# Performance work log

Hardware: AMD Instinct MI355X
Metric: run time of the kernel (lower is better)

Reference implementation:

```python
import jax, jax.numpy as jnp
import numpy as np

N = 4000; T_GRU = 32; T_TREE = 16; F = 256; HS = 128; H = 3 * HS; CC = 512; E = 64000; D4 = 4 * HS


def _gru_last(x, wi, wh, bi, bh):
    # x: [N, T, F]; torch GRU gate order r, z, n. Returns last hidden [N, H].
    xp = jnp.einsum('ntf,gf->ntg', x, wi) + bi  # [N, T, 3H]
    h0 = jnp.zeros((x.shape[0], wh.shape[1]), x.dtype)
    def step(h, xt):
        gh = h @ wh.T + bh
        ir, iz, inn = jnp.split(xt, 3, axis=1)
        hr, hz, hn = jnp.split(gh, 3, axis=1)
        r = jax.nn.sigmoid(ir + hr)
        z = jax.nn.sigmoid(iz + hz)
        n = jnp.tanh(inn + r * hn)
        return (1.0 - z) * n + z * h, None
    hT, _ = jax.lax.scan(step, h0, jnp.swapaxes(xp, 0, 1))
    return hT


def _tree_root(x, ioux_w, ioux_b, iouh_w, iouh_b, fx_w, fx_b, fh_w, fh_b):
    # Chain-structured TreeLSTM (each node has one child); x: [N, T, F], leaf-to-root.
    xi = jnp.einsum('ntf,gf->ntg', x, ioux_w) + ioux_b  # [N, T, 3M]
    xf = jnp.einsum('ntf,mf->ntm', x, fx_w) + fx_b      # [N, T, M]
    M = fh_w.shape[0]
    z0 = jnp.zeros((x.shape[0], M), x.dtype)
    def step(carry, xs):
        c, h = carry
        xi_t, xf_t = xs
        iou = xi_t + h @ iouh_w.T + iouh_b
        i, o, u = jnp.split(iou, 3, axis=1)
        f = jax.nn.sigmoid(xf_t + h @ fh_w.T + fh_b)
        c = jax.nn.sigmoid(i) * jnp.tanh(u) + f * c
        h = jax.nn.sigmoid(o) * jnp.tanh(c)
        return (c, h), None
    (c, h), _ = jax.lax.scan(step, (z0, z0), (jnp.swapaxes(xi, 0, 1), jnp.swapaxes(xf, 0, 1)))
    return h


def _gcn(x, w, b, row, col):
    # PyG GCNConv: self-loops + symmetric normalization.
    n = x.shape[0]
    xw = x @ w.T
    loops = jnp.arange(n, dtype=row.dtype)
    r = jnp.concatenate([row, loops])
    c = jnp.concatenate([col, loops])
    deg = jax.ops.segment_sum(jnp.ones(r.shape, x.dtype), c, num_segments=n)
    dinv = jnp.where(deg > 0, jax.lax.rsqrt(jnp.maximum(deg, 1e-12)), 0.0)
    norm = (dinv[r] * dinv[c])[:, None]
    return jax.ops.segment_sum(xw[r] * norm, c, num_segments=n) + b


def setup_inputs() -> dict:
    key = jax.random.key(0)
    ks = jax.random.split(key, 48)
    s = 0.05
    p = lambda i, sh: jax.random.normal(ks[i], sh, jnp.float32) * s
    return {
        'feat1': p(0, (N, T_GRU, F)),
        'feat2': p(1, (N, T_TREE, F)),
        'feat3': p(2, (N, T_TREE, F)),
        'feat4': p(3, (N, CC)),
        'edge_index': jax.random.randint(ks[4], (2, E), 0, N),
        'gru_wi': p(5, (3 * H, F)), 'gru_wh': p(6, (3 * H, H)),
        'gru_bi': p(7, (3 * H,)), 'gru_bh': p(8, (3 * H,)),
        't1_ioux_w': p(9, (3 * H, F)), 't1_ioux_b': p(10, (3 * H,)),
        't1_iouh_w': p(11, (3 * H, H)), 't1_iouh_b': p(12, (3 * H,)),
        't1_fx_w': p(13, (H, F)), 't1_fx_b': p(14, (H,)),
        't1_fh_w': p(15, (H, H)), 't1_fh_b': p(16, (H,)),
        't2_ioux_w': p(17, (3 * H, F)), 't2_ioux_b': p(18, (3 * H,)),
        't2_iouh_w': p(19, (3 * H, H)), 't2_iouh_b': p(20, (3 * H,)),
        't2_fx_w': p(21, (H, F)), 't2_fx_b': p(22, (H,)),
        't2_fh_w': p(23, (H, H)), 't2_fh_b': p(24, (H,)),
        'r1_w': p(25, (HS, H)), 'r1_b': p(26, (HS,)),
        'r2_w': p(27, (HS, H)), 'r2_b': p(28, (HS,)),
        'r3_w': p(29, (HS, H)), 'r3_b': p(30, (HS,)),
        'r4_w': p(31, (HS, CC)), 'r4_b': p(32, (HS,)),
        'gcn0_w': p(33, (D4, D4)), 'gcn0_b': p(34, (D4,)),
        'gcn1_w': p(35, (D4, D4)), 'gcn1_b': p(36, (D4,)),
        'r7_w': p(37, (2, D4)), 'r7_b': p(38, (2,)),
    }


def reference(feat1, feat2, feat3, feat4, edge_index,
              gru_wi, gru_wh, gru_bi, gru_bh,
              t1_ioux_w, t1_ioux_b, t1_iouh_w, t1_iouh_b, t1_fx_w, t1_fx_b, t1_fh_w, t1_fh_b,
              t2_ioux_w, t2_ioux_b, t2_iouh_w, t2_iouh_b, t2_fx_w, t2_fx_b, t2_fh_w, t2_fh_b,
              r1_w, r1_b, r2_w, r2_b, r3_w, r3_b, r4_w, r4_b,
              gcn0_w, gcn0_b, gcn1_w, gcn1_b, r7_w, r7_b):
    v1 = _gru_last(feat1, gru_wi, gru_wh, gru_bi, gru_bh)            # [N, H]
    v2 = _tree_root(feat2, t1_ioux_w, t1_ioux_b, t1_iouh_w, t1_iouh_b, t1_fx_w, t1_fx_b, t1_fh_w, t1_fh_b)
    v3 = _tree_root(feat3, t2_ioux_w, t2_ioux_b, t2_iouh_w, t2_iouh_b, t2_fx_w, t2_fx_b, t2_fh_w, t2_fh_b)
    f1 = v1 @ r1_w.T + r1_b
    f2 = v2 @ r2_w.T + r2_b
    f3 = v3 @ r3_w.T + r3_b
    f4 = feat4 @ r4_w.T + r4_b
    m = jnp.concatenate([f1, f2, f3, f4], axis=1)                    # [N, 4*HS]
    row, col = edge_index[0], edge_index[1]
    m = jax.nn.relu(_gcn(m, gcn0_w, gcn0_b, row, col))
    m = _gcn(m, gcn1_w, gcn1_b, row, col)
    m = jax.nn.softmax(m @ r7_w.T + r7_b, axis=1)                    # [N, 2]
    return m.T                                                       # [2, N]
```

## Files before the change

### kernel.cpp

```cpp
#include <hip/hip_runtime.h>
#include <hip/hip_bf16.h>
#include <math.h>

#define NN 4000
#define TG 32
#define TT 16
#define FF 256
#define HH 384
#define GCOLS 1536
#define KCAT 640
#define EE 64000
#define D4 512

typedef __attribute__((ext_vector_type(8))) short short8;
typedef __attribute__((ext_vector_type(4))) float float4v;

static __device__ __forceinline__ float fsig(float x)  { return 1.0f / (1.0f + __expf(-x)); }
static __device__ __forceinline__ float ftanh(float x) { return 2.0f / (1.0f + __expf(-2.0f*x)) - 1.0f; }
static __device__ __forceinline__ unsigned short f2bf(float f) {
    __hip_bfloat16 h = __float2bfloat16(f); return *reinterpret_cast<unsigned short*>(&h);
}

static __device__ __forceinline__ void async_copy16(const void* g, void* l) {
    __builtin_amdgcn_global_load_lds(
        (const __attribute__((address_space(1))) unsigned int*)g,
        (__attribute__((address_space(3))) unsigned int*)l, 16, 0, 0);
}

static __device__ __forceinline__ void xcd_swz(int& bx, int& by, int& bz) {
    const int gx = gridDim.x, gy = gridDim.y;
    const int nwg = gx * gy * gridDim.z;
    const int w = (blockIdx.z * gy + blockIdx.y) * gx + blockIdx.x;
    const int q = nwg >> 3, r = nwg & 7;
    const int xcd = w & 7, i = w >> 3;
    const int L = (xcd < r ? xcd*(q+1) : r*(q+1) + (xcd - r)*q) + i;
    bx = L % gx; int rest = L / gx;
    by = rest % gy; bz = rest / gy;
}

__global__ __launch_bounds__(256) void prep_w_kernel(
    const float* __restrict__ gwi, const float* __restrict__ gwh,
    const float* __restrict__ gbi, const float* __restrict__ gbh,
    const float* __restrict__ x1w, const float* __restrict__ x1b,
    const float* __restrict__ h1w, const float* __restrict__ h1b,
    const float* __restrict__ fx1w, const float* __restrict__ fx1b,
    const float* __restrict__ fh1w, const float* __restrict__ fh1b,
    const float* __restrict__ x2w, const float* __restrict__ x2b,
    const float* __restrict__ h2w, const float* __restrict__ h2b,
    const float* __restrict__ fx2w, const float* __restrict__ fx2b,
    const float* __restrict__ fh2w, const float* __restrict__ fh2b,
    __hip_bfloat16* __restrict__ Wx, __hip_bfloat16* __restrict__ Wh,
    float* __restrict__ bp)
{
    int z = blockIdx.z;
    int idx = blockIdx.x * 256 + threadIdx.x;
    int c = idx / KCAT, k = idx - c * KCAT;
    int bx = c >> 7, wc = (c >> 6) & 1, g = (c >> 4) & 3, rl = c & 15;
    int j = bx*32 + wc*16 + rl;
    float v = 0.0f, bv = 0.0f;
    if (z == 0) {
        if (g <= 1) {
            int row = g*HH + j;
            v = (k < FF) ? gwi[row*FF + k] : gwh[row*HH + (k-FF)];
            bv = gbi[row] + gbh[row];
        } else if (g == 2) {
            int row = 2*HH + j;
            v = (k < FF) ? gwi[row*FF + k] : 0.0f;
            bv = gbi[row];
        } else {
            int row = 2*HH + j;
            v = (k < FF) ? 0.0f : gwh[row*HH + (k-FF)];
            bv = gbh[row];
        }
    } else {
        const float* xw  = (z==1)? x1w  : x2w;   const float* xb  = (z==1)? x1b  : x2b;
        const float* hw  = (z==1)? h1w  : h2w;   const float* hb_ = (z==1)? h1b  : h2b;
        const float* fxw = (z==1)? fx1w : fx2w;  const float* fxb = (z==1)? fx1b : fx2b;
        const float* fhw = (z==1)? fh1w : fh2w;  const float* fhb = (z==1)? fh1b : fh2b;
        if (g < 3) {
            int row = g*HH + j;
            v = (k < FF) ? xw[row*FF + k] : hw[row*HH + (k-FF)];
            bv = xb[row] + hb_[row];
        } else {
            v = (k < FF) ? fxw[j*FF + k] : fhw[j*HH + (k-FF)];
            bv = fxb[j] + fhb[j];
        }
    }
    if (k < FF) Wx[(size_t)z*GCOLS*FF + (size_t)c*FF + k] = __float2bfloat16(v);
    else        Wh[(size_t)z*GCOLS*HH + (size_t)c*HH + (k-FF)] = __float2bfloat16(v);
    if (k == 0) bp[z*GCOLS + c] = bv;
}

__global__ __launch_bounds__(256) void f2b4_kernel(const float* __restrict__ s,
                                                   __hip_bfloat16* __restrict__ d, int n4)
{
    int i = blockIdx.x*256 + threadIdx.x;
    if (i >= n4) return;
    float4 v = ((const float4*)s)[i];
    ushort4 u = { f2bf(v.x), f2bf(v.y), f2bf(v.z), f2bf(v.w) };
    ((ushort4*)d)[i] = u;
}

#define BM 128
#define BN 128
#define BKK 32

__global__ __launch_bounds__(256) void gemm0_k(
    const __hip_bfloat16* __restrict__ Ab, size_t zA, int lda,
    const __hip_bfloat16* __restrict__ Wb, size_t zW, int K,
    const float* __restrict__ bias, size_t zB,
    float* __restrict__ C, size_t zC,
    __hip_bfloat16* __restrict__ C16, size_t zC16,
    int ldC, int M)
{
    const int z = blockIdx.z;
    const __hip_bfloat16* A = Ab + zA*z;
    const __hip_bfloat16* W = Wb + zW*z;

    __shared__ __align__(16) __hip_bfloat16 As[BM][BKK];
    __shared__ __align__(16) __hip_bfloat16 Bs[BN][BKK];

    const int tid  = threadIdx.x;
    const int lane = tid & 63;
    const int w    = tid >> 6;
    const int wr = w >> 1, wc = w & 1;
    const int rowBase = blockIdx.y * BM;
    const int colBase = blockIdx.x * BN;
    const int sRow = tid >> 2;
    const int sK   = (tid & 3) * 8;

    float4v acc[4][4];
    #pragma unroll
    for (int i = 0; i < 4; ++i)
        #pragma unroll
        for (int j = 0; j < 4; ++j)
            acc[i][j] = (float4v){0.f, 0.f, 0.f, 0.f};

    const int rl = lane & 15;
    const int kl = (lane >> 4) * 8;

    for (int kt = 0; kt < K; kt += BKK) {
        const int kk = kt + sK;
        #pragma unroll
        for (int i = 0; i < 2; ++i) {
            int gr = rowBase + i*64 + sRow;
            if (gr > M-1) gr = M-1;
            async_copy16(A + (size_t)gr*lda + kk, &As[i*64 + sRow][sK]);
        }
        #pragma unroll
        for (int i = 0; i < 2; ++i) {
            int r = i*64 + sRow;
            async_copy16(W + (size_t)(colBase + r)*K + kk, &Bs[r][sK]);
        }
        __syncthreads();

        short8 af[4], bfr[4];
        #pragma unroll
        for (int mi = 0; mi < 4; ++mi)
            af[mi] = *(const short8*)&As[wr*64 + mi*16 + rl][kl];
        #pragma unroll
        for (int ni = 0; ni < 4; ++ni)
            bfr[ni] = *(const short8*)&Bs[wc*64 + ni*16 + rl][kl];
        #pragma unroll
        for (int mi = 0; mi < 4; ++mi)
            #pragma unroll
            for (int ni = 0; ni < 4; ++ni)
                acc[mi][ni] = __builtin_amdgcn_mfma_f32_16x16x32_bf16(af[mi], bfr[ni], acc[mi][ni], 0, 0, 0);
        __syncthreads();
    }

    const int rq = (lane >> 4) * 4;
    float* Cz = C + zC*z;
    __hip_bfloat16* C16z = C16 ? (C16 + zC16*z) : nullptr;
    #pragma unroll
    for (int mi = 0; mi < 4; ++mi) {
        #pragma unroll
        for (int q = 0; q < 4; ++q) {
            int row = rowBase + wr*64 + mi*16 + rq + q;
            if (row >= M) continue;
            #pragma unroll
            for (int ni = 0; ni < 4; ++ni) {
                int col = colBase + wc*64 + ni*16 + rl;
                float v = acc[mi][ni][q];
                if (bias) v += bias[zB*z + col];
                Cz[(size_t)row*ldC + col] = v;
                if (C16z) C16z[(size_t)row*ldC + col] = __float2bfloat16(v);
            }
        }
    }
}

#define SBM 64
#define NT (KCAT/BKK)

struct StepSet {
    const __hip_bfloat16 *X, *Hin, *Wx, *Wh;
    const float *bp, *Sin;
    float *Sout;
    __hip_bfloat16 *Hout;
    int lda, xoff;
};

template<int MODE>
__global__ __launch_bounds__(256) void step_k(StepSet G, StepSet T)
{
    int bxi, byi, bzi;
    xcd_swz(bxi, byi, bzi);

    int mode, zt;
    if (MODE == 3 && bzi > 0) { mode = 2; zt = bzi - 1; }
    else { mode = 1; zt = 0; }
    const StepSet& S = (mode == 1) ? G : T;

    const __hip_bfloat16* X  = S.X   + (size_t)zt*TT*NN*FF;
    const __hip_bfloat16* Hi = S.Hin + (size_t)zt*NN*HH;
    const __hip_bfloat16* Wx = S.Wx  + (size_t)zt*GCOLS*FF;
    const __hip_bfloat16* Wh = S.Wh  + (size_t)zt*GCOLS*HH;
    const float* bp = S.bp + (size_t)zt*GCOLS;
    const float* Si = S.Sin + (size_t)zt*NN*HH;
    float* So = S.Sout + (size_t)zt*NN*HH;
    __hip_bfloat16* Ho = S.Hout + (size_t)zt*NN*HH;
    const int lda = S.lda, xoff = S.xoff;

    __shared__ __align__(16) __hip_bfloat16 As[4][SBM][BKK];
    __shared__ __align__(16) __hip_bfloat16 Bs[4][BN][BKK];

    const int tid  = threadIdx.x;
    const int lane = tid & 63;
    const int w    = tid >> 6;
    const int wr = w >> 1, wc = w & 1;
    const int rowBase = byi * SBM;
    const int colBase = bxi * BN;

    const int sR  = tid >> 2;
    const int sC  = tid & 3;
    const int sSw = sC ^ ((sR >> 1) & 3);
    int gra = rowBase + sR; if (gra > NN-1) gra = NN-1;

    auto stage = [&](int buf, int kt) {
        if (kt < FF) {
            const int kk = kt + sSw*8;
            async_copy16(X  + (size_t)gra*lda + xoff + kk,          &As[buf][sR][sC*8]);
            async_copy16(Wx + (size_t)(colBase + sR)*FF + kk,       &Bs[buf][sR][sC*8]);
            async_copy16(Wx + (size_t)(colBase + 64 + sR)*FF + kk,  &Bs[buf][64 + sR][sC*8]);
        } else {
            const int kk = kt - FF + sSw*8;
            async_copy16(Hi + (size_t)gra*HH + kk,                  &As[buf][sR][sC*8]);
            async_copy16(Wh + (size_t)(colBase + sR)*HH + kk,       &Bs[buf][sR][sC*8]);
            async_copy16(Wh + (size_t)(colBase + 64 + sR)*HH + kk,  &Bs[buf][64 + sR][sC*8]);
        }
    };

    float4v acc[2][4];
    #pragma unroll
    for (int i = 0; i < 2; ++i)
        #pragma unroll
        for (int j = 0; j < 4; ++j)
            acc[i][j] = (float4v){0.f, 0.f, 0.f, 0.f};

    const int rl = lane & 15;
    const int dF = (lane >> 4) ^ ((rl >> 1) & 3);

    stage(0, 0);
    stage(1, BKK);

    for (int it = 0; it < NT; ++it) {
        if (it < NT-1) asm volatile("s_waitcnt vmcnt(3)" ::: "memory");
        else           asm volatile("s_waitcnt vmcnt(0)" ::: "memory");
        __builtin_amdgcn_sched_barrier(0);
        __builtin_amdgcn_s_barrier();
        __builtin_amdgcn_sched_barrier(0);
        if (it + 2 < NT) stage((it+2)&3, (it+2)*BKK);
        __builtin_amdgcn_sched_barrier(0);

        const int cur = it & 3;
        short8 af[2], bfr[4];
        #pragma unroll
        for (int mi = 0; mi < 2; ++mi)
            af[mi] = *(const short8*)&As[cur][wr*32 + mi*16 + rl][dF*8];

        const bool xph = (it*BKK) < FF;
        if (mode == 2) {
            #pragma unroll
            for (int ni = 0; ni < 4; ++ni)
                bfr[ni] = *(const short8*)&Bs[cur][wc*64 + ni*16 + rl][dF*8];
            asm volatile("s_waitcnt lgkmcnt(0)" ::: "memory");
            __builtin_amdgcn_sched_barrier(0);
            #pragma unroll
            for (int mi = 0; mi < 2; ++mi)
                #pragma unroll
                for (int ni = 0; ni < 4; ++ni)
                    acc[mi][ni] = __builtin_amdgcn_mfma_f32_16x16x32_bf16(af[mi], bfr[ni], acc[mi][ni], 0, 0, 0);
        } else if (xph) {
            #pragma unroll
            for (int ni = 0; ni < 3; ++ni)
                bfr[ni] = *(const short8*)&Bs[cur][wc*64 + ni*16 + rl][dF*8];
            asm volatile("s_waitcnt lgkmcnt(0)" ::: "memory");
            __builtin_amdgcn_sched_barrier(0);
            #pragma unroll
            for (int mi = 0; mi < 2; ++mi)
                #pragma unroll
                for (int ni = 0; ni < 3; ++ni)
                    acc[mi][ni] = __builtin_amdgcn_mfma_f32_16x16x32_bf16(af[mi], bfr[ni], acc[mi][ni], 0, 0, 0);
        } else {
            bfr[0] = *(const short8*)&Bs[cur][wc*64 + 0*16 + rl][dF*8];
            bfr[1] = *(const short8*)&Bs[cur][wc*64 + 1*16 + rl][dF*8];
            bfr[3] = *(const short8*)&Bs[cur][wc*64 + 3*16 + rl][dF*8];
            asm volatile("s_waitcnt lgkmcnt(0)" ::: "memory");
            __builtin_amdgcn_sched_barrier(0);
            #pragma unroll
            for (int mi = 0; mi < 2; ++mi) {
                acc[mi][0] = __builtin_amdgcn_mfma_f32_16x16x32_bf16(af[mi], bfr[0], acc[mi][0], 0, 0, 0);
                acc[mi][1] = __builtin_amdgcn_mfma_f32_16x16x32_bf16(af[mi], bfr[1], acc[mi][1], 0, 0, 0);
                acc[mi][3] = __builtin_amdgcn_mfma_f32_16x16x32_bf16(af[mi], bfr[3], acc[mi][3], 0, 0, 0);
            }
        }
    }

    const int rq = (lane >> 4) * 4;
    const int j  = (colBase >> 2) + wc*16 + rl;
    const int cb = colBase + wc*64 + rl;
    float b0 = bp[cb + 0];
    float b1 = bp[cb + 16];
    float b2 = bp[cb + 32];
    float b3 = bp[cb + 48];

    #pragma unroll
    for (int mi = 0; mi < 2; ++mi) {
        #pragma unroll
        for (int q = 0; q < 4; ++q) {
            int row = rowBase + wr*32 + mi*16 + rq + q;
            if (row >= NN) continue;
            float g0 = acc[mi][0][q] + b0;
            float g1 = acc[mi][1][q] + b1;
            float g2 = acc[mi][2][q] + b2;
            float g3 = acc[mi][3][q] + b3;
            size_t off = (size_t)row*HH + j;
            if (mode == 1) {
                float r  = fsig(g0), zz = fsig(g1);
                float n  = ftanh(g2 + r*g3);
                float hp = Si[off];
                float hn = (1.0f - zz)*n + zz*hp;
                So[off] = hn;
                Ho[off] = __float2bfloat16(hn);
            } else {
                float cp = Si[off];
                float cn = fsig(g0)*ftanh(g2) + fsig(g3)*cp;
                So[off] = cn;
                float hn = fsig(g1)*ftanh(cn);
                Ho[off] = __float2bfloat16(hn);
            }
        }
    }
}

__global__ __launch_bounds__(256) void count_kernel(const int* __restrict__ col, int* __restrict__ degi)
{
    int e = blockIdx.x*256 + threadIdx.x;
    if (e < EE) atomicAdd(&degi[col[e]], 1);
}

__global__ __launch_bounds__(1024) void scan_kernel(const int* __restrict__ degi,
    int* __restrict__ start, int* __restrict__ cursor, float* __restrict__ dinv)
{
    __shared__ int s[1024];
    int t = threadIdx.x;
    int v[4]; int sum = 0;
    #pragma unroll
    for (int i = 0; i < 4; ++i) {
        int idx = t*4 + i;
        v[i] = (idx < NN) ? degi[idx] : 0;
        sum += v[i];
    }
    s[t] = sum;
    __syncthreads();
    for (int d = 1; d < 1024; d <<= 1) {
        int x = (t >= d) ? s[t-d] : 0;
        __syncthreads();
        s[t] += x;
        __syncthreads();
    }
    int base = s[t] - sum;
    int run = 0;
    #pragma unroll
    for (int i = 0; i < 4; ++i) {
        int idx = t*4 + i;
        if (idx < NN) {
            int st = base + run;
            start[idx] = st;
            cursor[idx] = st;
            dinv[idx] = rsqrtf((float)v[i] + 1.0f);
        }
        run += v[i];
    }
    if (t == 1023) start[NN] = s[1023];
}

__global__ __launch_bounds__(256) void fill_kernel(const int* __restrict__ row,
    const int* __restrict__ col, int* __restrict__ cursor, int* __restrict__ esrc)
{
    int e = blockIdx.x*256 + threadIdx.x;
    if (e < EE) {
        int c = col[e];
        int pos = atomicAdd(&cursor[c], 1);
        esrc[pos] = row[e];
    }
}

__global__ __launch_bounds__(256) void gather_kernel(const float* __restrict__ xw,
    const int* __restrict__ esrc, const int* __restrict__ start,
    const float* __restrict__ dinv, const float* __restrict__ bias,
    float* __restrict__ mout, __hip_bfloat16* __restrict__ mout16, int relu)
{
    int wv = threadIdx.x >> 6, lane = threadIdx.x & 63;
    int n = blockIdx.x*4 + wv;
    if (n >= NN) return;
    float a[8] = {0.f,0.f,0.f,0.f,0.f,0.f,0.f,0.f};
    int s0 = start[n], s1 = start[n+1];
    float dn = dinv[n];
    for (int e = s0; e < s1; ++e) {
        int r = esrc[e];
        float nrm = dinv[r]*dn;
        const float4 v0 = *(const float4*)(xw + (size_t)r*D4 + lane*8);
        const float4 v1 = *(const float4*)(xw + (size_t)r*D4 + lane*8 + 4);
        a[0] += v0.x*nrm; a[1] += v0.y*nrm; a[2] += v0.z*nrm; a[3] += v0.w*nrm;
        a[4] += v1.x*nrm; a[5] += v1.y*nrm; a[6] += v1.z*nrm; a[7] += v1.w*nrm;
    }
    const float4 u0 = *(const float4*)(xw + (size_t)n*D4 + lane*8);
    const float4 u1 = *(const float4*)(xw + (size_t)n*D4 + lane*8 + 4);
    float dd = dn*dn;
    float su[8] = {u0.x,u0.y,u0.z,u0.w,u1.x,u1.y,u1.z,u1.w};
    #pragma unroll
    for (int i = 0; i < 8; ++i) {
        float vv = a[i] + su[i]*dd + bias[lane*8 + i];
        if (relu) vv = fmaxf(vv, 0.0f);
        mout[(size_t)n*D4 + lane*8 + i] = vv;
        if (mout16) mout16[(size_t)n*D4 + lane*8 + i] = __float2bfloat16(vv);
    }
}

__global__ __launch_bounds__(256) void final_kernel(const float* __restrict__ m,
    const float* __restrict__ w, const float* __restrict__ b, float* __restrict__ out)
{
    int wave = threadIdx.x >> 6;
    int lane = threadIdx.x & 63;
    int n = blockIdx.x*4 + wave;
    const float* row = m + (size_t)n*D4 + lane*8;
    float4 v0 = *(const float4*)(row);
    float4 v1 = *(const float4*)(row + 4);
    const float* w0 = w + lane*8;
    const float* w1 = w + D4 + lane*8;
    float4 u0 = *(const float4*)(w0); float4 u1 = *(const float4*)(w0 + 4);
    float4 t0 = *(const float4*)(w1); float4 t1 = *(const float4*)(w1 + 4);
    float a = v0.x*u0.x + v0.y*u0.y + v0.z*u0.z + v0.w*u0.w
            + v1.x*u1.x + v1.y*u1.y + v1.z*u1.z + v1.w*u1.w;
    float bb = v0.x*t0.x + v0.y*t0.y + v0.z*t0.z + v0.w*t0.w
             + v1.x*t1.x + v1.y*t1.y + v1.z*t1.z + v1.w*t1.w;
    #pragma unroll
    for (int s = 32; s; s >>= 1) { a += __shfl_xor(a, s); bb += __shfl_xor(bb, s); }
    if (lane == 0) {
        float l0 = a + b[0], l1 = bb + b[1];
        float mx = fmaxf(l0, l1);
        float e0 = expf(l0 - mx), e1 = expf(l1 - mx);
        float s = e0 + e1;
        out[n]      = e0 / s;
        out[NN + n] = e1 / s;
    }
}

extern "C" void kernel_launch(void* const* d_in, const int* in_sizes, int n_in,
                              void* d_out, int out_size, void* d_ws, size_t ws_size,
                              hipStream_t stream)
{
    const float* feat1 = (const float*)d_in[0];
    const float* feat2 = (const float*)d_in[1];
    const float* feat3 = (const float*)d_in[2];
    const float* feat4 = (const float*)d_in[3];
    const int*   eidx  = (const int*)d_in[4];
    const float* r1w = (const float*)d_in[25]; const float* r1b = (const float*)d_in[26];
    const float* r2w = (const float*)d_in[27]; const float* r2b = (const float*)d_in[28];
    const float* r3w = (const float*)d_in[29]; const float* r3b = (const float*)d_in[30];
    const float* r4w = (const float*)d_in[31]; const float* r4b = (const float*)d_in[32];
    const float* g0w = (const float*)d_in[33]; const float* g0b = (const float*)d_in[34];
    const float* g1w = (const float*)d_in[35]; const float* g1b = (const float*)d_in[36];
    const float* r7w = (const float*)d_in[37]; const float* r7b = (const float*)d_in[38];

    float* ws = (float*)d_ws;
    size_t o = 0;
    auto alloc = [&](size_t nfl) { float* p = ws + o; o += (nfl + 3) & ~(size_t)3; return p; };

    float* hf0 = alloc((size_t)NN*HH);
    float* cf0 = alloc((size_t)2*NN*HH);
    __hip_bfloat16* hb0 = (__hip_bfloat16*)alloc((size_t)3*NN*HH/2);
    size_t zeroFloats = o;
    float* hf1 = alloc((size_t)NN*HH);
    float* cf1 = alloc((size_t)2*NN*HH);
    __hip_bfloat16* hb1 = (__hip_bfloat16*)alloc((size_t)3*NN*HH/2);
    __hip_bfloat16* xg  = (__hip_bfloat16*)alloc((size_t)TG*NN*FF/2);
    __hip_bfloat16* xt  = (__hip_bfloat16*)alloc((size_t)2*TT*NN*FF/2);
    __hip_bfloat16* Wx  = (__hip_bfloat16*)alloc((size_t)3*GCOLS*FF/2);
    __hip_bfloat16* Wh  = (__hip_bfloat16*)alloc((size_t)3*GCOLS*HH/2);
    float* bp   = alloc(3*GCOLS);
    float* mbuf = alloc((size_t)NN*D4);
    float* xwb  = alloc((size_t)NN*D4);
    float* dinv = alloc(NN);
    __hip_bfloat16* mbf16 = (__hip_bfloat16*)alloc((size_t)NN*D4/2);
    __hip_bfloat16* f4b   = (__hip_bfloat16*)alloc((size_t)NN*D4/2);
    __hip_bfloat16* rw123 = (__hip_bfloat16*)alloc((size_t)3*128*HH/2);
    float* rb123 = alloc(3*128);
    __hip_bfloat16* r4w16 = (__hip_bfloat16*)alloc((size_t)128*D4/2);
    __hip_bfloat16* g0w16 = (__hip_bfloat16*)alloc((size_t)D4*D4/2);
    __hip_bfloat16* g1w16 = (__hip_bfloat16*)alloc((size_t)D4*D4/2);
    int* degi   = (int*)alloc(NN);
    int* start  = (int*)alloc(NN + 4);
    int* cursor = (int*)alloc(NN);
    int* esrc   = (int*)alloc(EE);

    float* hfp[2] = {hf0, hf1};
    float* cfp[2] = {cf0, cf1};
    __hip_bfloat16* hbp[2] = {hb0, hb1};

    hipMemsetAsync(hf0, 0, zeroFloats*sizeof(float), stream);
    hipMemsetAsync(degi, 0, NN*sizeof(int), stream);

    prep_w_kernel<<<dim3(3840,1,3),256,0,stream>>>(
        (const float*)d_in[5],(const float*)d_in[6],(const float*)d_in[7],(const float*)d_in[8],
        (const float*)d_in[9],(const float*)d_in[10],(const float*)d_in[11],(const float*)d_in[12],
        (const float*)d_in[13],(const float*)d_in[14],(const float*)d_in[15],(const float*)d_in[16],
        (const float*)d_in[17],(const float*)d_in[18],(const float*)d_in[19],(const float*)d_in[20],
        (const float*)d_in[21],(const float*)d_in[22],(const float*)d_in[23],(const float*)d_in[24],
        Wx, Wh, bp);

    f2b4_kernel<<<32000,256,0,stream>>>(feat1, xg, TG*NN*FF/4);
    f2b4_kernel<<<16000,256,0,stream>>>(feat2, xt, TT*NN*FF/4);
    f2b4_kernel<<<16000,256,0,stream>>>(feat3, xt + (size_t)TT*NN*FF, TT*NN*FF/4);
    f2b4_kernel<<<2000,256,0,stream>>>(feat4, f4b, NN*D4/4);
    f2b4_kernel<<<48,256,0,stream>>>(r1w, rw123, 128*HH/4);
    f2b4_kernel<<<48,256,0,stream>>>(r2w, rw123 + 128*HH, 128*HH/4);
    f2b4_kernel<<<48,256,0,stream>>>(r3w, rw123 + 2*128*HH, 128*HH/4);
    f2b4_kernel<<<64,256,0,stream>>>(r4w, r4w16, 128*D4/4);
    f2b4_kernel<<<256,256,0,stream>>>(g0w, g0w16, D4*D4/4);
    f2b4_kernel<<<256,256,0,stream>>>(g1w, g1w16, D4*D4/4);
    hipMemcpyAsync(rb123,       r1b, 128*sizeof(float), hipMemcpyDeviceToDevice, stream);
    hipMemcpyAsync(rb123 + 128, r2b, 128*sizeof(float), hipMemcpyDeviceToDevice, stream);
    hipMemcpyAsync(rb123 + 256, r3b, 128*sizeof(float), hipMemcpyDeviceToDevice, stream);

    count_kernel<<<250,256,0,stream>>>(eidx + EE, degi);
    scan_kernel<<<1,1024,0,stream>>>(degi, start, cursor, dinv);
    fill_kernel<<<250,256,0,stream>>>(eidx, eidx + EE, cursor, esrc);

    for (int t = 0; t < TT; ++t) {
        int p = t & 1, q = p ^ 1;
        StepSet Gs = { xg, hbp[p], Wx, Wh, bp, hfp[p], hfp[q], hbp[q], TG*FF, t*FF };
        StepSet Ts = { xt, hbp[p] + (size_t)NN*HH,
                       Wx + (size_t)GCOLS*FF, Wh + (size_t)GCOLS*HH,
                       bp + GCOLS, cfp[p], cfp[q],
                       hbp[q] + (size_t)NN*HH, TT*FF, t*FF };
        step_k<3><<<dim3(GCOLS/BN, 63, 3),256,0,stream>>>(Gs, Ts);
    }
    for (int t = TT; t < TG; ++t) {
        int p = t & 1, q = p ^ 1;
        StepSet Gs = { xg, hbp[p], Wx, Wh, bp, hfp[p], hfp[q], hbp[q], TG*FF, t*FF };
        step_k<1><<<dim3(GCOLS/BN, 63, 1),256,0,stream>>>(Gs, Gs);
    }

    gemm0_k<<<dim3(1,32,3),256,0,stream>>>(
        hbp[0], (size_t)NN*HH, HH, rw123, (size_t)128*HH, HH, rb123, 128,
        mbuf, 128, mbf16, 128, D4, NN);
    gemm0_k<<<dim3(1,32,1),256,0,stream>>>(
        f4b, 0, D4, r4w16, 0, D4, r4b, 0,
        mbuf + 384, 0, mbf16 + 384, 0, D4, NN);

    gemm0_k<<<dim3(4,32,1),256,0,stream>>>(
        mbf16, 0, D4, g0w16, 0, D4, nullptr, 0,
        xwb, 0, nullptr, 0, D4, NN);
    gather_kernel<<<1000,256,0,stream>>>(xwb, esrc, start, dinv, g0b, mbuf, mbf16, 1);

    gemm0_k<<<dim3(4,32,1),256,0,stream>>>(
        mbf16, 0, D4, g1w16, 0, D4, nullptr, 0,
        xwb, 0, nullptr, 0, D4, NN);
    gather_kernel<<<1000,256,0,stream>>>(xwb, esrc, start, dinv, g1b, mbuf, nullptr, 0);

    final_kernel<<<1000,256,0,stream>>>(mbuf, r7w, r7b, (float*)d_out);
}
```

Before: 1.547 ms.

## Split fused GRU/TreeLSTM step kernel into separate kernels with larger tree tiles

Replaces the combined per-step launch, which ran GRU and both TreeLSTM chains together for 16 steps, with 32 GRU-only launches followed by 16 launches of a dedicated TreeLSTM kernel. The tree kernel uses 128x128 tiles with a 3-stage buffer and 4x4 MFMA per warp, so there are fewer blocks and more reuse per loaded tile. It also removes the runtime mode branch from the GRU kernel. The tradeoff is losing the concurrency between GRU and tree work in the first 16 steps, which may leave the GPU underfilled because the tree grid is only 12x32x2 blocks.

```diff
diff --git a/kernel.cpp b/kernel.cpp
--- a/kernel.cpp
+++ b/kernel.cpp
@@ -190,9 +190,6 @@
     }
 }
 
-#define SBM 64
-#define NT (KCAT/BKK)
-
 struct StepSet {
     const __hip_bfloat16 *X, *Hin, *Wx, *Wh;
     const float *bp, *Sin;
@@ -201,25 +198,23 @@
     int lda, xoff;
 };
 
-template<int MODE>
-__global__ __launch_bounds__(256) void step_k(StepSet G, StepSet T)
+#define NT (KCAT/BKK)
+
+#define SBM 64
+
+__global__ __launch_bounds__(256) void step_k(StepSet S)
 {
     int bxi, byi, bzi;
     xcd_swz(bxi, byi, bzi);
 
-    int mode, zt;
-    if (MODE == 3 && bzi > 0) { mode = 2; zt = bzi - 1; }
-    else { mode = 1; zt = 0; }
-    const StepSet& S = (mode == 1) ? G : T;
-
-    const __hip_bfloat16* X  = S.X   + (size_t)zt*TT*NN*FF;
-    const __hip_bfloat16* Hi = S.Hin + (size_t)zt*NN*HH;
-    const __hip_bfloat16* Wx = S.Wx  + (size_t)zt*GCOLS*FF;
-    const __hip_bfloat16* Wh = S.Wh  + (size_t)zt*GCOLS*HH;
-    const float* bp = S.bp + (size_t)zt*GCOLS;
-    const float* Si = S.Sin + (size_t)zt*NN*HH;
-    float* So = S.Sout + (size_t)zt*NN*HH;
-    __hip_bfloat16* Ho = S.Hout + (size_t)zt*NN*HH;
+    const __hip_bfloat16* X  = S.X;
+    const __hip_bfloat16* Hi = S.Hin;
+    const __hip_bfloat16* Wx = S.Wx;
+    const __hip_bfloat16* Wh = S.Wh;
+    const float* bp = S.bp;
+    const float* Si = S.Sin;
+    float* So = S.Sout;
+    __hip_bfloat16* Ho = S.Hout;
     const int lda = S.lda, xoff = S.xoff;
 
     __shared__ __align__(16) __hip_bfloat16 As[4][SBM][BKK];
@@ -280,18 +275,7 @@
             af[mi] = *(const short8*)&As[cur][wr*32 + mi*16 + rl][dF*8];
 
         const bool xph = (it*BKK) < FF;
-        if (mode == 2) {
-            #pragma unroll
-            for (int ni = 0; ni < 4; ++ni)
-                bfr[ni] = *(const short8*)&Bs[cur][wc*64 + ni*16 + rl][dF*8];
-            asm volatile("s_waitcnt lgkmcnt(0)" ::: "memory");
-            __builtin_amdgcn_sched_barrier(0);
-            #pragma unroll
-            for (int mi = 0; mi < 2; ++mi)
-                #pragma unroll
-                for (int ni = 0; ni < 4; ++ni)
-                    acc[mi][ni] = __builtin_amdgcn_mfma_f32_16x16x32_bf16(af[mi], bfr[ni], acc[mi][ni], 0, 0, 0);
-        } else if (xph) {
+        if (xph) {
             #pragma unroll
             for (int ni = 0; ni < 3; ++ni)
                 bfr[ni] = *(const short8*)&Bs[cur][wc*64 + ni*16 + rl][dF*8];
@@ -336,20 +320,130 @@
             float g2 = acc[mi][2][q] + b2;
             float g3 = acc[mi][3][q] + b3;
             size_t off = (size_t)row*HH + j;
-            if (mode == 1) {
-                float r  = fsig(g0), zz = fsig(g1);
-                float n  = ftanh(g2 + r*g3);
-                float hp = Si[off];
-                float hn = (1.0f - zz)*n + zz*hp;
-                So[off] = hn;
-                Ho[off] = __float2bfloat16(hn);
-            } else {
-                float cp = Si[off];
-                float cn = fsig(g0)*ftanh(g2) + fsig(g3)*cp;
-                So[off] = cn;
-                float hn = fsig(g1)*ftanh(cn);
-                Ho[off] = __float2bfloat16(hn);
-            }
+            float r  = fsig(g0), zz = fsig(g1);
+            float n  = ftanh(g2 + r*g3);
+            float hp = Si[off];
+            float hn = (1.0f - zz)*n + zz*hp;
+            So[off] = hn;
+            Ho[off] = __float2bfloat16(hn);
+        }
+    }
+}
+
+__global__ __launch_bounds__(256) void stepT_k(StepSet T)
+{
+    int bxi, byi, bzi;
+    xcd_swz(bxi, byi, bzi);
+    const int zt = bzi;
+
+    const __hip_bfloat16* X  = T.X   + (size_t)zt*TT*NN*FF;
+    const __hip_bfloat16* Hi = T.Hin + (size_t)zt*NN*HH;
+    const __hip_bfloat16* Wx = T.Wx  + (size_t)zt*GCOLS*FF;
+    const __hip_bfloat16* Wh = T.Wh  + (size_t)zt*GCOLS*HH;
+    const float* bp = T.bp + (size_t)zt*GCOLS;
+    const float* Si = T.Sin + (size_t)zt*NN*HH;
+    float* So = T.Sout + (size_t)zt*NN*HH;
+    __hip_bfloat16* Ho = T.Hout + (size_t)zt*NN*HH;
+    const int lda = T.lda, xoff = T.xoff;
+
+    __shared__ __align__(16) __hip_bfloat16 As[3][BM][BKK];
+    __shared__ __align__(16) __hip_bfloat16 Bs[3][BN][BKK];
+
+    const int tid  = threadIdx.x;
+    const int lane = tid & 63;
+    const int w    = tid >> 6;
+    const int wr = w >> 1, wc = w & 1;
+    const int rowBase = byi * BM;
+    const int colBase = bxi * BN;
+
+    const int sR  = tid >> 2;
+    const int sC  = tid & 3;
+    const int sSw = sC ^ ((sR >> 1) & 3);
+    int gra0 = rowBase + sR;      if (gra0 > NN-1) gra0 = NN-1;
+    int gra1 = rowBase + 64 + sR; if (gra1 > NN-1) gra1 = NN-1;
+
+    auto stage = [&](int buf, int kt) {
+        if (kt < FF) {
+            const int kk = kt + sSw*8;
+            async_copy16(X  + (size_t)gra0*lda + xoff + kk,         &As[buf][sR][sC*8]);
+            async_copy16(X  + (size_t)gra1*lda + xoff + kk,         &As[buf][64 + sR][sC*8]);
+            async_copy16(Wx + (size_t)(colBase + sR)*FF + kk,       &Bs[buf][sR][sC*8]);
+            async_copy16(Wx + (size_t)(colBase + 64 + sR)*FF + kk,  &Bs[buf][64 + sR][sC*8]);
+        } else {
+            const int kk = kt - FF + sSw*8;
+            async_copy16(Hi + (size_t)gra0*HH + kk,                 &As[buf][sR][sC*8]);
+            async_copy16(Hi + (size_t)gra1*HH + kk,                 &As[buf][64 + sR][sC*8]);
+            async_copy16(Wh + (size_t)(colBase + sR)*HH + kk,       &Bs[buf][sR][sC*8]);
+            async_copy16(Wh + (size_t)(colBase + 64 + sR)*HH + kk,  &Bs[buf][64 + sR][sC*8]);
+        }
+    };
+
+    float4v acc[4][4];
+    #pragma unroll
+    for (int i = 0; i < 4; ++i)
+        #pragma unroll
+        for (int j = 0; j < 4; ++j)
+            acc[i][j] = (float4v){0.f, 0.f, 0.f, 0.f};
+
+    const int rl = lane & 15;
+    const int dF = (lane >> 4) ^ ((rl >> 1) & 3);
+
+    stage(0, 0);
+    stage(1, BKK);
+    int cur = 0, nx2 = 2;
+
+    for (int it = 0; it < NT; ++it) {
+        if (it < NT-1) asm volatile("s_waitcnt vmcnt(4)" ::: "memory");
+        else           asm volatile("s_waitcnt vmcnt(0)" ::: "memory");
+        __builtin_amdgcn_sched_barrier(0);
+        __builtin_amdgcn_s_barrier();
+        __builtin_amdgcn_sched_barrier(0);
+        if (it + 2 < NT) stage(nx2, (it+2)*BKK);
+        __builtin_amdgcn_sched_barrier(0);
+
+        short8 af[4], bfr[4];
+        #pragma unroll
+        for (int mi = 0; mi < 4; ++mi)
+            af[mi] = *(const short8*)&As[cur][wr*64 + mi*16 + rl][dF*8];
+        #pragma unroll
+        for (int ni = 0; ni < 4; ++ni)
+            bfr[ni] = *(const short8*)&Bs[cur][wc*64 + ni*16 + rl][dF*8];
+        asm volatile("s_waitcnt lgkmcnt(0)" ::: "memory");
+        __builtin_amdgcn_sched_barrier(0);
+        #pragma unroll
+        for (int mi = 0; mi < 4; ++mi)
+            #pragma unroll
+            for (int ni = 0; ni < 4; ++ni)
+                acc[mi][ni] = __builtin_amdgcn_mfma_f32_16x16x32_bf16(af[mi], bfr[ni], acc[mi][ni], 0, 0, 0);
+
+        cur = (cur == 2) ? 0 : cur + 1;
+        nx2 = (nx2 == 2) ? 0 : nx2 + 1;
+    }
+
+    const int rq = (lane >> 4) * 4;
+    const int j  = (colBase >> 2) + wc*16 + rl;
+    const int cb = colBase + wc*64 + rl;
+    float b0 = bp[cb + 0];
+    float b1 = bp[cb + 16];
+    float b2 = bp[cb + 32];
+    float b3 = bp[cb + 48];
+
+    #pragma unroll
+    for (int mi = 0; mi < 4; ++mi) {
+        #pragma unroll
+        for (int q = 0; q < 4; ++q) {
+            int row = rowBase + wr*64 + mi*16 + rq + q;
+            if (row >= NN) continue;
+            float g0 = acc[mi][0][q] + b0;
+            float g1 = acc[mi][1][q] + b1;
+            float g2 = acc[mi][2][q] + b2;
+            float g3 = acc[mi][3][q] + b3;
+            size_t off = (size_t)row*HH + j;
+            float cp = Si[off];
+            float cn = fsig(g0)*ftanh(g2) + fsig(g3)*cp;
+            So[off] = cn;
+            float hn = fsig(g1)*ftanh(cn);
+            Ho[off] = __float2bfloat16(hn);
         }
     }
 }
@@ -549,19 +643,18 @@
     scan_kernel<<<1,1024,0,stream>>>(degi, start, cursor, dinv);
     fill_kernel<<<250,256,0,stream>>>(eidx, eidx + EE, cursor, esrc);
 
+    for (int t = 0; t < TG; ++t) {
+        int p = t & 1, q = p ^ 1;
+        StepSet Gs = { xg, hbp[p], Wx, Wh, bp, hfp[p], hfp[q], hbp[q], TG*FF, t*FF };
+        step_k<<<dim3(GCOLS/BN, 63, 1),256,0,stream>>>(Gs);
+    }
     for (int t = 0; t < TT; ++t) {
         int p = t & 1, q = p ^ 1;
-        StepSet Gs = { xg, hbp[p], Wx, Wh, bp, hfp[p], hfp[q], hbp[q], TG*FF, t*FF };
         StepSet Ts = { xt, hbp[p] + (size_t)NN*HH,
                        Wx + (size_t)GCOLS*FF, Wh + (size_t)GCOLS*HH,
                        bp + GCOLS, cfp[p], cfp[q],
                        hbp[q] + (size_t)NN*HH, TT*FF, t*FF };
-        step_k<3><<<dim3(GCOLS/BN, 63, 3),256,0,stream>>>(Gs, Ts);
-    }
-    for (int t = TT; t < TG; ++t) {
-        int p = t & 1, q = p ^ 1;
-        StepSet Gs = { xg, hbp[p], Wx, Wh, bp, hfp[p], hfp[q], hbp[q], TG*FF, t*FF };
-        step_k<1><<<dim3(GCOLS/BN, 63, 1),256,0,stream>>>(Gs, Gs);
+        stepT_k<<<dim3(GCOLS/BN, 32, 2),256,0,stream>>>(Ts);
     }
 
     gemm0_k<<<dim3(1,32,3),256,0,stream>>>(
```

Result: faster. 1.398 ms (-9.6%).

## Split fused GRU/TreeLSTM step launches into separate mode-specialized kernels

Applied to the files above, without the earlier changes.

Each combined launch used to run the GRU step and both TreeLSTM chains together via the grid z dimension, with a runtime mode branch. Now all 32 GRU steps run first as their own launches, followed by separate launches for each tree chain at every tree step. The step kernel takes a single StepSet and picks its mode at compile time, which removes per-block branching and pointer offset arithmetic. The cost is twice as many launches, each with a smaller grid, so the GPU may be less full and tail effects may grow.

```diff
diff --git a/kernel.cpp b/kernel.cpp
--- a/kernel.cpp
+++ b/kernel.cpp
@@ -190,9 +190,6 @@
     }
 }
 
-#define SBM 64
-#define NT (KCAT/BKK)
-
 struct StepSet {
     const __hip_bfloat16 *X, *Hin, *Wx, *Wh;
     const float *bp, *Sin;
@@ -201,25 +198,23 @@
     int lda, xoff;
 };
 
+#define NT (KCAT/BKK)
+#define SBM 64
+
 template<int MODE>
-__global__ __launch_bounds__(256) void step_k(StepSet G, StepSet T)
+__global__ __launch_bounds__(256) void step_k(StepSet S)
 {
     int bxi, byi, bzi;
     xcd_swz(bxi, byi, bzi);
 
-    int mode, zt;
-    if (MODE == 3 && bzi > 0) { mode = 2; zt = bzi - 1; }
-    else { mode = 1; zt = 0; }
-    const StepSet& S = (mode == 1) ? G : T;
-
-    const __hip_bfloat16* X  = S.X   + (size_t)zt*TT*NN*FF;
-    const __hip_bfloat16* Hi = S.Hin + (size_t)zt*NN*HH;
-    const __hip_bfloat16* Wx = S.Wx  + (size_t)zt*GCOLS*FF;
-    const __hip_bfloat16* Wh = S.Wh  + (size_t)zt*GCOLS*HH;
-    const float* bp = S.bp + (size_t)zt*GCOLS;
-    const float* Si = S.Sin + (size_t)zt*NN*HH;
-    float* So = S.Sout + (size_t)zt*NN*HH;
-    __hip_bfloat16* Ho = S.Hout + (size_t)zt*NN*HH;
+    const __hip_bfloat16* X  = S.X;
+    const __hip_bfloat16* Hi = S.Hin;
+    const __hip_bfloat16* Wx = S.Wx;
+    const __hip_bfloat16* Wh = S.Wh;
+    const float* bp = S.bp;
+    const float* Si = S.Sin;
+    float* So = S.Sout;
+    __hip_bfloat16* Ho = S.Hout;
     const int lda = S.lda, xoff = S.xoff;
 
     __shared__ __align__(16) __hip_bfloat16 As[4][SBM][BKK];
@@ -280,7 +275,7 @@
             af[mi] = *(const short8*)&As[cur][wr*32 + mi*16 + rl][dF*8];
 
         const bool xph = (it*BKK) < FF;
-        if (mode == 2) {
+        if (MODE == 2) {
             #pragma unroll
             for (int ni = 0; ni < 4; ++ni)
                 bfr[ni] = *(const short8*)&Bs[cur][wc*64 + ni*16 + rl][dF*8];
@@ -336,7 +331,7 @@
             float g2 = acc[mi][2][q] + b2;
             float g3 = acc[mi][3][q] + b3;
             size_t off = (size_t)row*HH + j;
-            if (mode == 1) {
+            if (MODE == 1) {
                 float r  = fsig(g0), zz = fsig(g1);
                 float n  = ftanh(g2 + r*g3);
                 float hp = Si[off];
@@ -549,19 +544,25 @@
     scan_kernel<<<1,1024,0,stream>>>(degi, start, cursor, dinv);
     fill_kernel<<<250,256,0,stream>>>(eidx, eidx + EE, cursor, esrc);
 
+    for (int t = 0; t < TG; ++t) {
+        int p = t & 1, q = p ^ 1;
+        StepSet Gs = { xg, hbp[p], Wx, Wh, bp, hfp[p], hfp[q], hbp[q], TG*FF, t*FF };
+        step_k<1><<<dim3(GCOLS/BN, 63, 1),256,0,stream>>>(Gs);
+    }
     for (int t = 0; t < TT; ++t) {
         int p = t & 1, q = p ^ 1;
-        StepSet Gs = { xg, hbp[p], Wx, Wh, bp, hfp[p], hfp[q], hbp[q], TG*FF, t*FF };
-        StepSet Ts = { xt, hbp[p] + (size_t)NN*HH,
-                       Wx + (size_t)GCOLS*FF, Wh + (size_t)GCOLS*HH,
-                       bp + GCOLS, cfp[p], cfp[q],
-                       hbp[q] + (size_t)NN*HH, TT*FF, t*FF };
-        step_k<3><<<dim3(GCOLS/BN, 63, 3),256,0,stream>>>(Gs, Ts);
-    }
-    for (int t = TT; t < TG; ++t) {
-        int p = t & 1, q = p ^ 1;
-        StepSet Gs = { xg, hbp[p], Wx, Wh, bp, hfp[p], hfp[q], hbp[q], TG*FF, t*FF };
-        step_k<1><<<dim3(GCOLS/BN, 63, 1),256,0,stream>>>(Gs, Gs);
+        for (int tr = 0; tr < 2; ++tr) {
+            StepSet Ts = { xt + (size_t)tr*TT*NN*FF,
+                           hbp[p] + (size_t)(1+tr)*NN*HH,
+                           Wx + (size_t)(1+tr)*GCOLS*FF,
+                           Wh + (size_t)(1+tr)*GCOLS*HH,
+                           bp + (size_t)(1+tr)*GCOLS,
+                           cfp[p] + (size_t)tr*NN*HH,
+                           cfp[q] + (size_t)tr*NN*HH,
+                           hbp[q] + (size_t)(1+tr)*NN*HH,
+                           TT*FF, t*FF };
+            step_k<2><<<dim3(GCOLS/BN, 63, 1),256,0,stream>>>(Ts);
+        }
     }
 
     gemm0_k<<<dim3(1,32,3),256,0,stream>>>(
```

New measurement: 1.571 ms. Within noise of the previous version (+1.6%).
